# Optimization experiments

Measured on AMD Instinct MI355X. Metric: run time of the kernel, lower is better.

The kernel has to match this reference:

```python
import jax, jax.numpy as jnp
import numpy as np
import math

B, S, HID = 2, 1024, 2048
NH, HD = 16, 128
STREAM_R, SELECT_R, RECENT_R = 0.02, 0.06, 0.08
FF = 0.9  # forgetting factor
ROPE_BASE = 10000.0


def setup_inputs() -> dict:
    key = jax.random.key(0)
    ks = jax.random.split(key, 5)
    return {
        "hidden_states": jax.random.normal(ks[0], (B, S, HID), dtype=jnp.float32),
        "wq": jax.random.normal(ks[1], (HID, HID), dtype=jnp.float32) * 0.02,
        "wk": jax.random.normal(ks[2], (HID, HID), dtype=jnp.float32) * 0.02,
        "wv": jax.random.normal(ks[3], (HID, HID), dtype=jnp.float32) * 0.02,
        "wo": jax.random.normal(ks[4], (HID, HID), dtype=jnp.float32) * 0.02,
    }


def _rope_tables(seq_len, dim):
    inv_freq = 1.0 / (ROPE_BASE ** (jnp.arange(0, dim, 2, dtype=jnp.float32) / dim))
    freqs = jnp.outer(jnp.arange(seq_len, dtype=jnp.float32), inv_freq)  # [S, D/2]
    emb = jnp.concatenate([freqs, freqs], axis=-1)  # [S, D]
    return jnp.cos(emb), jnp.sin(emb)


def _rotate_half(x):
    x1, x2 = jnp.split(x, 2, axis=-1)
    return jnp.concatenate([-x2, x1], axis=-1)


def a2s_base_mask(attn_weights, sb, selb, rb, ff):
    # attn_weights: [B,H,S,S] (causal mask already added). Returns bool keep-mask [B,H,S,S].
    Bv, Hv, Sq, Sk = attn_weights.shape
    scores = jax.nn.softmax(attn_weights.astype(jnp.float32), axis=-1)  # [B,H,S,S]
    cb = sb + selb + rb  # cache budget
    # EMA warmup over first cb rows: sum_i ff^(cb-1-i) * scores[i]
    w = ff ** jnp.arange(cb - 1, -1, -1, dtype=jnp.float32)
    select0 = jnp.einsum('t,bhts->bhs', w, scores[:, :, :cb, :])
    mask0 = jnp.ones((Bv, Hv, Sk), dtype=bool)
    pos = jnp.arange(Sk)

    xs_scores = jnp.moveaxis(scores[:, :, cb:Sk - 1, :], 2, 0)  # [T,B,H,S]
    ts = jnp.arange(cb, Sk - 1, dtype=jnp.int32)

    def step(carry, inp):
        sel, m = carry
        sc, t = inp
        cur = sc * m
        cur = cur / jnp.sum(cur, axis=-1, keepdims=True)
        sel = ff * sel + cur
        local = t - rb
        # argmin over window [sb : local+1]; outside -> +inf (evicted entries already +inf)
        win = jnp.where((pos >= sb) & (pos <= local), sel, jnp.inf)
        mi = jnp.argmin(win, axis=-1)  # [B,H], first-min like torch
        evict = pos == mi[..., None]  # [B,H,S] one-hot bool
        sel = jnp.where(evict, jnp.inf, sel)
        m_new = m & ~evict
        return (sel, m_new), m_new

    _, rows = jax.lax.scan(step, (select0, mask0), (xs_scores, ts))
    head = jnp.ones((Bv, Hv, cb + 1, Sk), dtype=bool)  # rows 0..cb stay all-True
    tail = jnp.moveaxis(rows, 0, 2)  # rows cb+1..S-1
    return jnp.concatenate([head, tail], axis=2)


def reference(hidden_states, wq, wk, wv, wo):
    sb = math.floor(STREAM_R * S + 0.5)
    selb = math.floor(SELECT_R * S + 0.5)
    rb = math.floor(RECENT_R * S + 0.5)

    q = (hidden_states @ wq).reshape(B, S, NH, HD).transpose(0, 2, 1, 3)
    k = (hidden_states @ wk).reshape(B, S, NH, HD).transpose(0, 2, 1, 3)
    v = (hidden_states @ wv).reshape(B, S, NH, HD).transpose(0, 2, 1, 3)

    cos, sin = _rope_tables(S, HD)  # [S,HD]
    q = q * cos + _rotate_half(q) * sin
    k = k * cos + _rotate_half(k) * sin

    attn = jnp.einsum('bhqd,bhkd->bhqk', q, k) / math.sqrt(HD)
    mask_val = jnp.finfo(jnp.float32).min
    causal = jnp.where(jnp.tril(jnp.ones((S, S), dtype=bool)), 0.0, mask_val)[None, None]
    attn = jnp.maximum(attn + causal, mask_val)

    keep = a2s_base_mask(jax.lax.stop_gradient(attn), sb, selb, rb, FF)
    attn = jnp.where(keep, attn, mask_val)  # torch.min(attention_mask) == mask_val

    probs = jax.nn.softmax(attn.astype(jnp.float32), axis=-1).astype(q.dtype)
    out = jnp.einsum('bhqk,bhkd->bhqd', probs, v)
    out = out.transpose(0, 2, 1, 3).reshape(B, S, HID)
    return out @ wo
```

## Files before the change

kernel.cpp:

```cpp
#include <hip/hip_runtime.h>
#include <math.h>

#define Bb    2
#define Ss    1024
#define HIDd  2048
#define NHh   16
#define HDd   128
#define SBc   20
#define SELBc 61
#define RBc   82
#define CBc   163
#define FFf   0.9f
#define MASKVAL (-3.4028234663852886e38f)
#define NBH   (Bb*NHh)
#define NROWS (NBH*Ss)

typedef __attribute__((ext_vector_type(8))) short short8;
typedef __attribute__((ext_vector_type(4))) float f32x4;

__device__ __forceinline__ unsigned short f2b(float f) {
    unsigned u = __float_as_uint(f);
    u = (u + 0x7FFFu + ((u >> 16) & 1u)) >> 16;
    return (unsigned short)u;
}
__device__ __forceinline__ float b2f(unsigned short h) {
    return __uint_as_float((unsigned)h << 16);
}

#if defined(__has_builtin)
#if __has_builtin(__builtin_amdgcn_global_load_lds)
#define USE_GLD 1
#endif
#endif

__device__ __forceinline__ void gload16(const void* g, void* l) {
#ifdef USE_GLD
    __builtin_amdgcn_global_load_lds(
        (const __attribute__((address_space(1))) void*)g,
        (__attribute__((address_space(3))) void*)l, 16, 0, 0);
#else
    *(short8*)l = *(const short8*)g;
#endif
}

__global__ __launch_bounds__(256) void conv_split(const float* __restrict__ x,
                                                  unsigned short* __restrict__ yh,
                                                  unsigned short* __restrict__ yl, int n4)
{
    int i = blockIdx.x * 256 + threadIdx.x;
    if (i >= n4) return;
    float4 v = ((const float4*)x)[i];
    ushort4 h, l;
    h.x = f2b(v.x); l.x = f2b(v.x - b2f(h.x));
    h.y = f2b(v.y); l.y = f2b(v.y - b2f(h.y));
    h.z = f2b(v.z); l.z = f2b(v.z - b2f(h.z));
    h.w = f2b(v.w); l.w = f2b(v.w - b2f(h.w));
    ((ushort4*)yh)[i] = h;
    ((ushort4*)yl)[i] = l;
}

__global__ __launch_bounds__(256) void tconv_all(const float* __restrict__ wq,
                                                 const float* __restrict__ wk,
                                                 const float* __restrict__ wv,
                                                 const float* __restrict__ wo,
                                                 unsigned short* __restrict__ wqth,
                                                 unsigned short* __restrict__ wqtl,
                                                 unsigned short* __restrict__ wkth,
                                                 unsigned short* __restrict__ wktl,
                                                 unsigned short* __restrict__ wvt,
                                                 unsigned short* __restrict__ wot)
{
    __shared__ float T[64][65];
    const int z = blockIdx.z;
    const float* W = (z == 0) ? wq : (z == 1) ? wk : (z == 2) ? wv : wo;
    int n0 = blockIdx.x * 64, k0 = blockIdx.y * 64;
    int tid = threadIdx.x;
    int rr = tid >> 4, cc = (tid & 15) * 4;
#pragma unroll
    for (int p = 0; p < 4; ++p) {
        int r = rr + p * 16;
        float4 x = *(const float4*)&W[(size_t)(k0 + r) * HIDd + n0 + cc];
        T[r][cc] = x.x; T[r][cc + 1] = x.y; T[r][cc + 2] = x.z; T[r][cc + 3] = x.w;
    }
    __syncthreads();
    if (z < 2) {
        unsigned short* Wth = z ? wkth : wqth;
        unsigned short* Wtl = z ? wktl : wqtl;
#pragma unroll
        for (int p = 0; p < 4; ++p) {
            int rn = rr + p * 16;
            float v0 = T[cc][rn], v1 = T[cc + 1][rn], v2 = T[cc + 2][rn], v3 = T[cc + 3][rn];
            ushort4 h, l;
            h.x = f2b(v0); l.x = f2b(v0 - b2f(h.x));
            h.y = f2b(v1); l.y = f2b(v1 - b2f(h.y));
            h.z = f2b(v2); l.z = f2b(v2 - b2f(h.z));
            h.w = f2b(v3); l.w = f2b(v3 - b2f(h.w));
            *(ushort4*)&Wth[(size_t)(n0 + rn) * HIDd + k0 + cc] = h;
            *(ushort4*)&Wtl[(size_t)(n0 + rn) * HIDd + k0 + cc] = l;
        }
    } else {
        unsigned short* Wt = (z == 2) ? wvt : wot;
#pragma unroll
        for (int p = 0; p < 4; ++p) {
            int rn = rr + p * 16;
            ushort4 o;
            o.x = f2b(T[cc][rn]);     o.y = f2b(T[cc + 1][rn]);
            o.z = f2b(T[cc + 2][rn]); o.w = f2b(T[cc + 3][rn]);
            *(ushort4*)&Wt[(size_t)(n0 + rn) * HIDd + k0 + cc] = o;
        }
    }
}

__global__ __launch_bounds__(256) void gemm_qkv(const unsigned short* __restrict__ hsh,
                                                const unsigned short* __restrict__ hsl,
                                                const unsigned short* __restrict__ wqth,
                                                const unsigned short* __restrict__ wqtl,
                                                const unsigned short* __restrict__ wkth,
                                                const unsigned short* __restrict__ wktl,
                                                const unsigned short* __restrict__ wvt,
                                                float* __restrict__ qf,
                                                float* __restrict__ kf,
                                                float* __restrict__ vf)
{
    __shared__ unsigned short AsH[128 * 32], AsL[128 * 32];
    __shared__ unsigned short BsH[128 * 32], BsL[128 * 32];
    const int tid = threadIdx.x;
    const int region = blockIdx.x >> 4;
    const int bn = (blockIdx.x & 15) * 128;
    const int bm = blockIdx.y * 128;
    const int K = HIDd;
    const int lane = tid & 63, wid = tid >> 6;
    const int wr = (wid >> 1) * 64, wc = (wid & 1) * 64;
    const int lm = lane & 15, lk = (lane >> 4) * 8;
    const int lr = (lane >> 4) * 4;

    f32x4 acc[4][4];
#pragma unroll
    for (int mi = 0; mi < 4; ++mi)
#pragma unroll
        for (int ni = 0; ni < 4; ++ni) acc[mi][ni] = 0.0f;

    if (region < 2) {
        const unsigned short* Bh = region ? wkth : wqth;
        const unsigned short* Bl = region ? wktl : wqtl;
        float* C = region ? kf : qf;
        for (int k0 = 0; k0 < K; k0 += 32) {
#pragma unroll
            for (int l = 0; l < 2; ++l) {
                int L = tid + l * 256;
                int row = L >> 2, c8 = (L & 3) * 8;
                size_t ga = (size_t)(bm + row) * K + k0 + c8;
                size_t gb = (size_t)(bn + row) * K + k0 + c8;
                gload16(&hsh[ga], &AsH[L * 8]);
                gload16(&hsl[ga], &AsL[L * 8]);
                gload16(&Bh[gb], &BsH[L * 8]);
                gload16(&Bl[gb], &BsL[L * 8]);
            }
            __syncthreads();
            short8 ah[4], al[4], bh[4], bl[4];
#pragma unroll
            for (int mi = 0; mi < 4; ++mi) {
                ah[mi] = *(short8*)&AsH[(wr + mi * 16 + lm) * 32 + lk];
                al[mi] = *(short8*)&AsL[(wr + mi * 16 + lm) * 32 + lk];
            }
#pragma unroll
            for (int ni = 0; ni < 4; ++ni) {
                bh[ni] = *(short8*)&BsH[(wc + ni * 16 + lm) * 32 + lk];
                bl[ni] = *(short8*)&BsL[(wc + ni * 16 + lm) * 32 + lk];
            }
#pragma unroll
            for (int mi = 0; mi < 4; ++mi)
#pragma unroll
                for (int ni = 0; ni < 4; ++ni) {
                    acc[mi][ni] = __builtin_amdgcn_mfma_f32_16x16x32_bf16(ah[mi], bh[ni], acc[mi][ni], 0, 0, 0);
                    acc[mi][ni] = __builtin_amdgcn_mfma_f32_16x16x32_bf16(ah[mi], bl[ni], acc[mi][ni], 0, 0, 0);
                    acc[mi][ni] = __builtin_amdgcn_mfma_f32_16x16x32_bf16(al[mi], bh[ni], acc[mi][ni], 0, 0, 0);
                }
            __syncthreads();
        }
#pragma unroll
        for (int mi = 0; mi < 4; ++mi)
#pragma unroll
            for (int ni = 0; ni < 4; ++ni)
#pragma unroll
                for (int r = 0; r < 4; ++r) {
                    int m = bm + wr + mi * 16 + lr + r;
                    int n = bn + wc + ni * 16 + lm;
                    int b_ = m / Ss, s_ = m % Ss;
                    int h_ = n / HDd, d_ = n % HDd;
                    C[(size_t)((b_ * NHh + h_) * Ss + s_) * HDd + d_] = acc[mi][ni][r];
                }
    } else {
        for (int k0 = 0; k0 < K; k0 += 32) {
#pragma unroll
            for (int l = 0; l < 2; ++l) {
                int L = tid + l * 256;
                int row = L >> 2, c8 = (L & 3) * 8;
                gload16(&hsh[(size_t)(bm + row) * K + k0 + c8], &AsH[L * 8]);
                gload16(&wvt[(size_t)(bn + row) * K + k0 + c8], &BsH[L * 8]);
            }
            __syncthreads();
            short8 af[4], bf[4];
#pragma unroll
            for (int mi = 0; mi < 4; ++mi) af[mi] = *(short8*)&AsH[(wr + mi * 16 + lm) * 32 + lk];
#pragma unroll
            for (int ni = 0; ni < 4; ++ni) bf[ni] = *(short8*)&BsH[(wc + ni * 16 + lm) * 32 + lk];
#pragma unroll
            for (int mi = 0; mi < 4; ++mi)
#pragma unroll
                for (int ni = 0; ni < 4; ++ni)
                    acc[mi][ni] = __builtin_amdgcn_mfma_f32_16x16x32_bf16(af[mi], bf[ni], acc[mi][ni], 0, 0, 0);
            __syncthreads();
        }
#pragma unroll
        for (int mi = 0; mi < 4; ++mi)
#pragma unroll
            for (int ni = 0; ni < 4; ++ni)
#pragma unroll
                for (int r = 0; r < 4; ++r) {
                    int m = bm + wr + mi * 16 + lr + r;
                    int n = bn + wc + ni * 16 + lm;
                    int b_ = m / Ss, s_ = m % Ss;
                    int h_ = n / HDd, d_ = n % HDd;
                    vf[(size_t)((b_ * NHh + h_) * Ss + s_) * HDd + d_] = acc[mi][ni][r];
                }
    }
}

__global__ __launch_bounds__(256) void gemm_bf16t(const unsigned short* __restrict__ A,
                                                  const unsigned short* __restrict__ Bt,
                                                  float* __restrict__ C,
                                                  int M, int N, int K)
{
    __shared__ unsigned short As[128 * 32];
    __shared__ unsigned short Bs[128 * 32];
    const int tid = threadIdx.x;
    const int bm = blockIdx.y * 128, bn = blockIdx.x * 128;
    const int lane = tid & 63, wid = tid >> 6;
    const int wr = (wid >> 1) * 64, wc = (wid & 1) * 64;
    const int lm = lane & 15, lk = (lane >> 4) * 8;

    f32x4 acc[4][4];
#pragma unroll
    for (int mi = 0; mi < 4; ++mi)
#pragma unroll
        for (int ni = 0; ni < 4; ++ni) acc[mi][ni] = 0.0f;

    for (int k0 = 0; k0 < K; k0 += 32) {
#pragma unroll
        for (int l = 0; l < 2; ++l) {
            int L = tid + l * 256;
            int row = L >> 2, c8 = (L & 3) * 8;
            gload16(&A[(size_t)(bm + row) * K + k0 + c8], &As[L * 8]);
            gload16(&Bt[(size_t)(bn + row) * K + k0 + c8], &Bs[L * 8]);
        }
        __syncthreads();
        short8 af[4], bf[4];
#pragma unroll
        for (int mi = 0; mi < 4; ++mi) af[mi] = *(short8*)&As[(wr + mi * 16 + lm) * 32 + lk];
#pragma unroll
        for (int ni = 0; ni < 4; ++ni) bf[ni] = *(short8*)&Bs[(wc + ni * 16 + lm) * 32 + lk];
#pragma unroll
        for (int mi = 0; mi < 4; ++mi)
#pragma unroll
            for (int ni = 0; ni < 4; ++ni)
                acc[mi][ni] = __builtin_amdgcn_mfma_f32_16x16x32_bf16(af[mi], bf[ni], acc[mi][ni], 0, 0, 0);
        __syncthreads();
    }
    const int lr = (lane >> 4) * 4;
#pragma unroll
    for (int mi = 0; mi < 4; ++mi)
#pragma unroll
        for (int ni = 0; ni < 4; ++ni)
#pragma unroll
            for (int r = 0; r < 4; ++r) {
                int m = bm + wr + mi * 16 + lr + r;
                int n = bn + wc + ni * 16 + lm;
                C[(size_t)m * N + n] = acc[mi][ni][r];
            }
}

__global__ __launch_bounds__(64) void rope_qk_split(const float* __restrict__ q,
                                                    const float* __restrict__ k,
                                                    unsigned short* __restrict__ qh,
                                                    unsigned short* __restrict__ ql,
                                                    unsigned short* __restrict__ kh,
                                                    unsigned short* __restrict__ kl)
{
    int idx = blockIdx.x;
    int s = idx % Ss;
    int d = threadIdx.x;
    float inv = powf(10000.0f, -2.0f * (float)d / 128.0f);
    float fr = (float)s * inv;
    float c = cosf(fr), sn = sinf(fr);
    size_t base = (size_t)idx * HDd;
    float q1 = q[base + d], q2 = q[base + d + 64];
    float k1 = k[base + d], k2 = k[base + d + 64];
    float qa = q1 * c - q2 * sn, qbv = q2 * c + q1 * sn;
    float ka = k1 * c - k2 * sn, kbv = k2 * c + k1 * sn;
    unsigned short h;
    h = f2b(qa);  qh[base + d]      = h; ql[base + d]      = f2b(qa  - b2f(h));
    h = f2b(qbv); qh[base + d + 64] = h; ql[base + d + 64] = f2b(qbv - b2f(h));
    h = f2b(ka);  kh[base + d]      = h; kl[base + d]      = f2b(ka  - b2f(h));
    h = f2b(kbv); kh[base + d + 64] = h; kl[base + d + 64] = f2b(kbv - b2f(h));
}

__global__ __launch_bounds__(256) void attn_qk_split(const unsigned short* __restrict__ qh,
                                                     const unsigned short* __restrict__ ql,
                                                     const unsigned short* __restrict__ kh,
                                                     const unsigned short* __restrict__ kl,
                                                     float* __restrict__ attn)
{
    const int bh = blockIdx.z;
    const int bm = blockIdx.y * 128, bn = blockIdx.x * 128;
    const int tid = threadIdx.x;

    if (blockIdx.x > blockIdx.y) return;

    float* C = attn + (size_t)bh * Ss * Ss;
    const size_t hb = (size_t)bh * Ss * HDd;
    const unsigned short* Ah = qh + hb;
    const unsigned short* Al = ql + hb;
    const unsigned short* Bh = kh + hb;
    const unsigned short* Bl = kl + hb;

    __shared__ unsigned short AsH[128 * 32], AsL[128 * 32];
    __shared__ unsigned short BsH[128 * 32], BsL[128 * 32];
    const int lane = tid & 63, wid = tid >> 6;
    const int wr = (wid >> 1) * 64, wc = (wid & 1) * 64;
    const int lm = lane & 15, lk = (lane >> 4) * 8;

    f32x4 acc[4][4];
#pragma unroll
    for (int mi = 0; mi < 4; ++mi)
#pragma unroll
        for (int ni = 0; ni < 4; ++ni) acc[mi][ni] = 0.0f;

    for (int k0 = 0; k0 < HDd; k0 += 32) {
#pragma unroll
        for (int l = 0; l < 2; ++l) {
            int L = tid + l * 256;
            int row = L >> 2, c8 = (L & 3) * 8;
            size_t ga = (size_t)(bm + row) * HDd + k0 + c8;
            size_t gb = (size_t)(bn + row) * HDd + k0 + c8;
            gload16(&Ah[ga], &AsH[L * 8]);
            gload16(&Al[ga], &AsL[L * 8]);
            gload16(&Bh[gb], &BsH[L * 8]);
            gload16(&Bl[gb], &BsL[L * 8]);
        }
        __syncthreads();
        short8 ah[4], al[4], bh2[4], bl2[4];
#pragma unroll
        for (int mi = 0; mi < 4; ++mi) {
            ah[mi] = *(short8*)&AsH[(wr + mi * 16 + lm) * 32 + lk];
            al[mi] = *(short8*)&AsL[(wr + mi * 16 + lm) * 32 + lk];
        }
#pragma unroll
        for (int ni = 0; ni < 4; ++ni) {
            bh2[ni] = *(short8*)&BsH[(wc + ni * 16 + lm) * 32 + lk];
            bl2[ni] = *(short8*)&BsL[(wc + ni * 16 + lm) * 32 + lk];
        }
#pragma unroll
        for (int mi = 0; mi < 4; ++mi)
#pragma unroll
            for (int ni = 0; ni < 4; ++ni) {
                acc[mi][ni] = __builtin_amdgcn_mfma_f32_16x16x32_bf16(ah[mi], bh2[ni], acc[mi][ni], 0, 0, 0);
                acc[mi][ni] = __builtin_amdgcn_mfma_f32_16x16x32_bf16(ah[mi], bl2[ni], acc[mi][ni], 0, 0, 0);
                acc[mi][ni] = __builtin_amdgcn_mfma_f32_16x16x32_bf16(al[mi], bh2[ni], acc[mi][ni], 0, 0, 0);
            }
        __syncthreads();
    }
    const float scale = 0.08838834764831845f;
    const int lr = (lane >> 4) * 4;
#pragma unroll
    for (int mi = 0; mi < 4; ++mi)
#pragma unroll
        for (int ni = 0; ni < 4; ++ni)
#pragma unroll
            for (int r = 0; r < 4; ++r) {
                int sq = bm + wr + mi * 16 + lr + r;
                int sk = bn + wc + ni * 16 + lm;
                C[(size_t)sq * Ss + sk] = (sk <= sq) ? acc[mi][ni][r] * scale : MASKVAL;
            }
}

__global__ __launch_bounds__(256) void softmax_rows(float* __restrict__ attn)
{
    int row = blockIdx.x;
    int r = row & (Ss - 1);
    float4* a4 = (float4*)(attn + (size_t)row * Ss);
    int tid = threadIdx.x;
    bool act = (tid * 4 <= r);
    float4 x = make_float4(MASKVAL, MASKVAL, MASKVAL, MASKVAL);
    if (act) x = a4[tid];
    float m = fmaxf(fmaxf(x.x, x.y), fmaxf(x.z, x.w));
#pragma unroll
    for (int off = 32; off; off >>= 1) m = fmaxf(m, __shfl_xor(m, off));
    __shared__ float red[4];
    if ((tid & 63) == 0) red[tid >> 6] = m;
    __syncthreads();
    float mm = fmaxf(fmaxf(red[0], red[1]), fmaxf(red[2], red[3]));
    float e0 = expf(x.x - mm), e1 = expf(x.y - mm);
    float e2 = expf(x.z - mm), e3 = expf(x.w - mm);
    float s = e0 + e1 + e2 + e3;
#pragma unroll
    for (int off = 32; off; off >>= 1) s += __shfl_xor(s, off);
    __shared__ float red2[4];
    if ((tid & 63) == 0) red2[tid >> 6] = s;
    __syncthreads();
    float inv = 1.0f / (red2[0] + red2[1] + red2[2] + red2[3]);
    a4[tid] = make_float4(e0 * inv, e1 * inv, e2 * inv, e3 * inv);
}

template<int CTRL>
__device__ __forceinline__ int dpp_i(int x) {
    return __builtin_amdgcn_update_dpp(0, x, CTRL, 0xF, 0xF, true);
}
__device__ __forceinline__ float wave_sum64(float x) {
    x += __int_as_float(dpp_i<0xB1>(__float_as_int(x)));
    x += __int_as_float(dpp_i<0x4E>(__float_as_int(x)));
    x += __int_as_float(dpp_i<0x141>(__float_as_int(x)));
    x += __int_as_float(dpp_i<0x140>(__float_as_int(x)));
    int xi = __float_as_int(x);
    float a = __int_as_float(__builtin_amdgcn_readlane(xi, 0));
    float b = __int_as_float(__builtin_amdgcn_readlane(xi, 16));
    float c = __int_as_float(__builtin_amdgcn_readlane(xi, 32));
    float d = __int_as_float(__builtin_amdgcn_readlane(xi, 48));
    return (a + c) + (b + d);
}

__device__ __forceinline__ unsigned long long u64min(unsigned long long a, unsigned long long b) {
    return a < b ? a : b;
}
template<int CTRL>
__device__ __forceinline__ unsigned long long dpp64(unsigned long long x) {
    int lo = (int)(unsigned)x;
    int hi = (int)(unsigned)(x >> 32);
    unsigned l2 = (unsigned)dpp_i<CTRL>(lo);
    unsigned h2 = (unsigned)dpp_i<CTRL>(hi);
    return ((unsigned long long)h2 << 32) | (unsigned long long)l2;
}
__device__ __forceinline__ unsigned long long wave_min64k(unsigned long long x) {
    x = u64min(x, dpp64<0xB1>(x));
    x = u64min(x, dpp64<0x4E>(x));
    x = u64min(x, dpp64<0x141>(x));
    x = u64min(x, dpp64<0x140>(x));
    int lo = (int)(unsigned)x;
    int hi = (int)(unsigned)(x >> 32);
    unsigned long long a = ((unsigned long long)(unsigned)__builtin_amdgcn_readlane(hi, 0)  << 32) |
                           (unsigned long long)(unsigned)__builtin_amdgcn_readlane(lo, 0);
    unsigned long long b = ((unsigned long long)(unsigned)__builtin_amdgcn_readlane(hi, 16) << 32) |
                           (unsigned long long)(unsigned)__builtin_amdgcn_readlane(lo, 16);
    unsigned long long c = ((unsigned long long)(unsigned)__builtin_amdgcn_readlane(hi, 32) << 32) |
                           (unsigned long long)(unsigned)__builtin_amdgcn_readlane(lo, 32);
    unsigned long long d = ((unsigned long long)(unsigned)__builtin_amdgcn_readlane(hi, 48) << 32) |
                           (unsigned long long)(unsigned)__builtin_amdgcn_readlane(lo, 48);
    return u64min(u64min(a, b), u64min(c, d));
}

__device__ __forceinline__ float f4c(float4 v, int i) {
    return i == 0 ? v.x : (i == 1 ? v.y : (i == 2 ? v.z : v.w));
}

template<int NC, int NCL>
__device__ __forceinline__ void scan_step(int t, int lane,
                                          const float4* __restrict__ A4,
                                          unsigned char* __restrict__ KP,
                                          float4 (&rb)[4],
                                          float (&sel)[4][4],
                                          float (&mf)[4][4])
{
    const float INFv = __int_as_float(0x7f800000);
    float4 a[NC];
#pragma unroll
    for (int jj = 0; jj < NC; ++jj) a[jj] = rb[jj];
    int tp = t + 4; if (tp > Ss - 1) tp = Ss - 1;
#pragma unroll
    for (int jj = 0; jj < NCL; ++jj) rb[jj] = A4[tp * 256 + jj * 64 + lane];

    float lsum = 0.0f;
#pragma unroll
    for (int jj = 0; jj < NC; ++jj) {
        float c0 = a[jj].x * mf[jj][0], c1 = a[jj].y * mf[jj][1];
        float c2 = a[jj].z * mf[jj][2], c3 = a[jj].w * mf[jj][3];
        lsum += (c0 + c1) + (c2 + c3);
    }
    float tot = wave_sum64(lsum);
    float inv = 1.0f / tot;

    const int local = t - RBc;
    const int base = lane * 4;
    const bool ge = (base >= SBc);

    unsigned long long kmin = 0xFFFFFFFFFFFFFFFFull;
#pragma unroll
    for (int jj = 0; jj < NC; ++jj) {
        unsigned long long kk[4];
#pragma unroll
        for (int i = 0; i < 4; ++i) {
            float sv = fmaf(FFf, sel[jj][i], f4c(a[jj], i) * inv);
            sel[jj][i] = sv;
            int s = jj * 256 + base + i;
            bool win = (s <= local) && (jj > 0 || ge);
            unsigned hi = win ? __float_as_uint(sv) : 0x7f800000u;
            kk[i] = ((unsigned long long)hi << 32) | (unsigned long long)(unsigned)s;
        }
        unsigned long long cm = u64min(u64min(kk[0], kk[1]), u64min(kk[2], kk[3]));
        kmin = u64min(kmin, cm);
    }
    kmin = wave_min64k(kmin);
    const int besti = (int)(unsigned)(kmin & 0xFFFFFFFFull);

#pragma unroll
    for (int jj = 0; jj < NC; ++jj)
#pragma unroll
        for (int i = 0; i < 4; ++i) {
            int s = jj * 256 + base + i;
            bool e = (s == besti);
            sel[jj][i] = e ? INFv : sel[jj][i];
            mf[jj][i]  = e ? 0.0f : mf[jj][i];
        }

    uchar4* kp4 = (uchar4*)(KP + (size_t)(t + 1) * Ss);
#pragma unroll
    for (int jj = 0; jj < NC; ++jj) {
        uchar4 kb;
        kb.x = (unsigned char)mf[jj][0];
        kb.y = (unsigned char)mf[jj][1];
        kb.z = (unsigned char)mf[jj][2];
        kb.w = (unsigned char)mf[jj][3];
        kp4[jj * 64 + lane] = kb;
    }
}

__global__ __launch_bounds__(64) void scan_kernel5(const float* __restrict__ scores,
                                                   unsigned char* __restrict__ keep)
{
    int bh = blockIdx.x;
    int lane = threadIdx.x;
    const float4* A4 = (const float4*)(scores + (size_t)bh * Ss * Ss);
    unsigned char* KP = keep + (size_t)bh * Ss * Ss;

    float sel[4][4];
    float mf[4][4];
#pragma unroll
    for (int jj = 0; jj < 4; ++jj)
#pragma unroll
        for (int i = 0; i < 4; ++i) { sel[jj][i] = 0.0f; mf[jj][i] = 1.0f; }

    float4 w0 = A4[0 * 256 + lane];
    float4 w1 = A4[1 * 256 + lane];
    float4 w2 = A4[2 * 256 + lane];
    float4 w3 = A4[3 * 256 + lane];
#define WSTEP(W, NEXT)                                                       \
    do {                                                                     \
        float4 _a = W;                                                       \
        W = A4[(NEXT) * 256 + lane];                                         \
        sel[0][0] = fmaf(FFf, sel[0][0], _a.x);                              \
        sel[0][1] = fmaf(FFf, sel[0][1], _a.y);                              \
        sel[0][2] = fmaf(FFf, sel[0][2], _a.z);                              \
        sel[0][3] = fmaf(FFf, sel[0][3], _a.w);                              \
    } while (0)
    for (int r = 0; r < 160; r += 4) {
        WSTEP(w0, r + 4); WSTEP(w1, r + 5); WSTEP(w2, r + 6); WSTEP(w3, r + 7);
    }
#undef WSTEP
    {
        float4 tl[3] = { w0, w1, w2 };
#pragma unroll
        for (int u = 0; u < 3; ++u) {
            sel[0][0] = fmaf(FFf, sel[0][0], tl[u].x);
            sel[0][1] = fmaf(FFf, sel[0][1], tl[u].y);
            sel[0][2] = fmaf(FFf, sel[0][2], tl[u].z);
            sel[0][3] = fmaf(FFf, sel[0][3], tl[u].w);
        }
    }

    float4 rb[4][4];
#pragma unroll
    for (int slot = 0; slot < 4; ++slot)
        rb[slot][0] = A4[(163 + slot) * 256 + lane];

    for (int t0 = 163; t0 < 255; t0 += 4) {
        scan_step<1, 2>(t0 + 0, lane, A4, KP, rb[0], sel, mf);
        scan_step<1, 2>(t0 + 1, lane, A4, KP, rb[1], sel, mf);
        scan_step<1, 2>(t0 + 2, lane, A4, KP, rb[2], sel, mf);
        scan_step<1, 2>(t0 + 3, lane, A4, KP, rb[3], sel, mf);
    }
    for (int t0 = 255; t0 < 511; t0 += 4) {
        scan_step<2, 3>(t0 + 0, lane, A4, KP, rb[0], sel, mf);
        scan_step<2, 3>(t0 + 1, lane, A4, KP, rb[1], sel, mf);
        scan_step<2, 3>(t0 + 2, lane, A4, KP, rb[2], sel, mf);
        scan_step<2, 3>(t0 + 3, lane, A4, KP, rb[3], sel, mf);
    }
    for (int t0 = 511; t0 < 767; t0 += 4) {
        scan_step<3, 4>(t0 + 0, lane, A4, KP, rb[0], sel, mf);
        scan_step<3, 4>(t0 + 1, lane, A4, KP, rb[1], sel, mf);
        scan_step<3, 4>(t0 + 2, lane, A4, KP, rb[2], sel, mf);
        scan_step<3, 4>(t0 + 3, lane, A4, KP, rb[3], sel, mf);
    }
    for (int t0 = 767; t0 < 1023; t0 += 4) {
        scan_step<4, 4>(t0 + 0, lane, A4, KP, rb[0], sel, mf);
        scan_step<4, 4>(t0 + 1, lane, A4, KP, rb[1], sel, mf);
        scan_step<4, 4>(t0 + 2, lane, A4, KP, rb[2], sel, mf);
        scan_step<4, 4>(t0 + 3, lane, A4, KP, rb[3], sel, mf);
    }
}

__global__ __launch_bounds__(256) void pv_renorm(const float* __restrict__ scores,
                                                 const unsigned char* __restrict__ keep,
                                                 const float* __restrict__ v,
                                                 unsigned short* __restrict__ ctxb)
{
    int bh = blockIdx.z;
    int b_ = bh / NHh, h_ = bh % NHh;
    const float* P = scores + (size_t)bh * Ss * Ss;
    const unsigned char* KPm = keep + (size_t)bh * Ss * Ss;
    const float* V = v + (size_t)bh * Ss * HDd;
    int bm = blockIdx.y * 64, bn = blockIdx.x * 64;
    int tid = threadIdx.x, tx = tid & 15, ty = tid >> 4;
    __shared__ float As[16][68];
    __shared__ float Bs[16][64];
    float acc[4][4] = {};
    float rs[4] = {};
    int kend = bm + 64;
    for (int k0 = 0; k0 < kend; k0 += 16) {
#pragma unroll
        for (int l = 0; l < 4; ++l) {
            int idx = tid + l * 256;
            int r = idx >> 4, c = idx & 15;
            int row = bm + r;
            float p = P[(size_t)row * Ss + k0 + c];
            if (row > CBc && !KPm[(size_t)row * Ss + k0 + c]) p = 0.0f;
            As[c][r] = p;
        }
#pragma unroll
        for (int l = 0; l < 4; ++l) {
            int idx = tid + l * 256;
            int r = idx >> 6, c = idx & 63;
            Bs[r][c] = V[(size_t)(k0 + r) * HDd + bn + c];
        }
        __syncthreads();
#pragma unroll
        for (int kk = 0; kk < 16; ++kk) {
            float4 av = *(const float4*)&As[kk][ty * 4];
            float4 bv = *(const float4*)&Bs[kk][tx * 4];
            float a[4] = { av.x, av.y, av.z, av.w };
            float b[4] = { bv.x, bv.y, bv.z, bv.w };
#pragma unroll
            for (int i = 0; i < 4; ++i) rs[i] += a[i];
#pragma unroll
            for (int i = 0; i < 4; ++i)
#pragma unroll
                for (int j = 0; j < 4; ++j)
                    acc[i][j] = fmaf(a[i], b[j], acc[i][j]);
        }
        __syncthreads();
    }
#pragma unroll
    for (int i = 0; i < 4; ++i) {
        float inv = 1.0f / rs[i];
        int sq = bm + ty * 4 + i;
#pragma unroll
        for (int j = 0; j < 4; ++j) {
            int d = bn + tx * 4 + j;
            ctxb[(size_t)(b_ * Ss + sq) * HIDd + h_ * HDd + d] = f2b(acc[i][j] * inv);
        }
    }
}

extern "C" void kernel_launch(void* const* d_in, const int* in_sizes, int n_in,
                              void* d_out, int out_size, void* d_ws, size_t ws_size,
                              hipStream_t stream)
{
    const float* hs = (const float*)d_in[0];
    const float* wq = (const float*)d_in[1];
    const float* wk = (const float*)d_in[2];
    const float* wv = (const float*)d_in[3];
    const float* wo = (const float*)d_in[4];
    float* out = (float*)d_out;

    float* ws = (float*)d_ws;
    size_t off = 0;
    float* qf   = ws + off; off += (size_t)NBH * Ss * HDd;
    float* kf   = ws + off; off += (size_t)NBH * Ss * HDd;
    float* vf   = ws + off; off += (size_t)NBH * Ss * HDd;
    float* attn = ws + off; off += (size_t)NBH * Ss * Ss;
    unsigned char* keep = (unsigned char*)(ws + off); off += (size_t)NBH * Ss * Ss / 4;
    unsigned short* wot = (unsigned short*)(ws + off); off += (size_t)HIDd * HIDd / 2;

    unsigned short* hsh  = (unsigned short*)(attn);
    unsigned short* hsl  = (unsigned short*)(attn + 2u * 1024 * 1024);
    unsigned short* wqth = (unsigned short*)(attn + 4u * 1024 * 1024);
    unsigned short* wqtl = (unsigned short*)(attn + 6u * 1024 * 1024);
    unsigned short* wkth = (unsigned short*)(attn + 8u * 1024 * 1024);
    unsigned short* wktl = (unsigned short*)(attn + 10u * 1024 * 1024);
    unsigned short* wvt  = (unsigned short*)(attn + 12u * 1024 * 1024);
    unsigned short* qh = (unsigned short*)keep;
    unsigned short* ql = (unsigned short*)(keep + 8u * 1024 * 1024);
    unsigned short* kh = (unsigned short*)(keep + 16u * 1024 * 1024);
    unsigned short* kl = (unsigned short*)(keep + 24u * 1024 * 1024);
    unsigned short* ctxb = (unsigned short*)qf;

    dim3 blk(256);
    const int M = Bb * Ss;

    conv_split<<<dim3((M * HIDd / 4 + 255) / 256), blk, 0, stream>>>(hs, hsh, hsl, M * HIDd / 4);

    tconv_all<<<dim3(HIDd / 64, HIDd / 64, 4), blk, 0, stream>>>(
        wq, wk, wv, wo, wqth, wqtl, wkth, wktl, wvt, wot);

    gemm_qkv<<<dim3(48, M / 128), blk, 0, stream>>>(
        hsh, hsl, wqth, wqtl, wkth, wktl, wvt, qf, kf, vf);

    rope_qk_split<<<dim3(NBH * Ss), dim3(64), 0, stream>>>(qf, kf, qh, ql, kh, kl);

    attn_qk_split<<<dim3(Ss / 128, Ss / 128, NBH), blk, 0, stream>>>(qh, ql, kh, kl, attn);

    softmax_rows<<<dim3(NROWS), blk, 0, stream>>>(attn);

    scan_kernel5<<<dim3(NBH), dim3(64), 0, stream>>>(attn, keep);

    pv_renorm<<<dim3(HDd / 64, Ss / 64, NBH), blk, 0, stream>>>(attn, keep, vf, ctxb);

    gemm_bf16t<<<dim3(HIDd / 128, M / 128), blk, 0, stream>>>(ctxb, wot, out, M, HIDd, HIDd);
}
```

Before: 974.9 us.

## Fuse RoPE and bf16 hi/lo split into QKV GEMM epilogue; skip masked diagonal MFMAs

The Q/K projection GEMM now applies rotary embedding and writes the bf16 high/low split directly in its epilogue. The two head-dim halves are exchanged through shared memory, so the fp32 q/k intermediates and the separate rope_qk_split launch go away. Separately, diagonal blocks of the QK^T kernel skip MFMA sub-tiles that lie entirely above the causal diagonal. This trades extra epilogue work and a barrier in the GEMM for less global memory traffic and one fewer launch. Only half the warps do the rope epilogue, which may leave the other half idle.

Result: slower. 1.434 ms (+47.1%).

```diff
diff --git a/kernel.cpp b/kernel.cpp
--- a/kernel.cpp
+++ b/kernel.cpp
@@ -118,12 +118,17 @@
                                                 const unsigned short* __restrict__ wkth,
                                                 const unsigned short* __restrict__ wktl,
                                                 const unsigned short* __restrict__ wvt,
-                                                float* __restrict__ qf,
-                                                float* __restrict__ kf,
+                                                unsigned short* __restrict__ qhp,
+                                                unsigned short* __restrict__ qlp,
+                                                unsigned short* __restrict__ khp,
+                                                unsigned short* __restrict__ klp,
                                                 float* __restrict__ vf)
 {
-    __shared__ unsigned short AsH[128 * 32], AsL[128 * 32];
-    __shared__ unsigned short BsH[128 * 32], BsL[128 * 32];
+    __shared__ unsigned short SM[4 * 128 * 32];
+    unsigned short* AsH = SM;
+    unsigned short* AsL = SM + 128 * 32;
+    unsigned short* BsH = SM + 2 * 128 * 32;
+    unsigned short* BsL = SM + 3 * 128 * 32;
     const int tid = threadIdx.x;
     const int region = blockIdx.x >> 4;
     const int bn = (blockIdx.x & 15) * 128;
@@ -143,7 +148,6 @@
     if (region < 2) {
         const unsigned short* Bh = region ? wkth : wqth;
         const unsigned short* Bl = region ? wktl : wqtl;
-        float* C = region ? kf : qf;
         for (int k0 = 0; k0 < K; k0 += 32) {
 #pragma unroll
             for (int l = 0; l < 2; ++l) {
@@ -178,18 +182,53 @@
                 }
             __syncthreads();
         }
-#pragma unroll
-        for (int mi = 0; mi < 4; ++mi)
-#pragma unroll
-            for (int ni = 0; ni < 4; ++ni)
+        unsigned short* Ho = region ? khp : qhp;
+        unsigned short* Lo = region ? klp : qlp;
+        float* Lx = (float*)SM;
+        if (wc) {
+#pragma unroll
+            for (int mi = 0; mi < 4; ++mi)
+#pragma unroll
+                for (int ni = 0; ni < 4; ++ni)
+#pragma unroll
+                    for (int r = 0; r < 4; ++r) {
+                        int row = wr + mi * 16 + lr + r;
+                        int dc = ni * 16 + lm;
+                        Lx[row * 64 + dc] = acc[mi][ni][r];
+                    }
+        }
+        __syncthreads();
+        if (!wc) {
+            float invt[4];
+#pragma unroll
+            for (int ni = 0; ni < 4; ++ni) {
+                int d = ni * 16 + lm;
+                invt[ni] = powf(10000.0f, -2.0f * (float)d / 128.0f);
+            }
+            const int hh = bn >> 7;
+#pragma unroll
+            for (int mi = 0; mi < 4; ++mi)
 #pragma unroll
                 for (int r = 0; r < 4; ++r) {
-                    int m = bm + wr + mi * 16 + lr + r;
-                    int n = bn + wc + ni * 16 + lm;
-                    int b_ = m / Ss, s_ = m % Ss;
-                    int h_ = n / HDd, d_ = n % HDd;
-                    C[(size_t)((b_ * NHh + h_) * Ss + s_) * HDd + d_] = acc[mi][ni][r];
+                    int row = wr + mi * 16 + lr + r;
+                    int m = bm + row;
+                    int b_ = m >> 10, s_ = m & (Ss - 1);
+                    size_t gb = ((size_t)(b_ * NHh + hh) * Ss + s_) * HDd;
+#pragma unroll
+                    for (int ni = 0; ni < 4; ++ni) {
+                        int d = ni * 16 + lm;
+                        float q1 = acc[mi][ni][r];
+                        float q2 = Lx[row * 64 + d];
+                        float fr = (float)s_ * invt[ni];
+                        float c = cosf(fr), sn = sinf(fr);
+                        float qa  = q1 * c - q2 * sn;
+                        float qbv = q2 * c + q1 * sn;
+                        unsigned short h;
+                        h = f2b(qa);  Ho[gb + d]      = h; Lo[gb + d]      = f2b(qa  - b2f(h));
+                        h = f2b(qbv); Ho[gb + d + 64] = h; Lo[gb + d + 64] = f2b(qbv - b2f(h));
+                    }
                 }
+        }
     } else {
         for (int k0 = 0; k0 < K; k0 += 32) {
 #pragma unroll
@@ -280,31 +319,6 @@
             }
 }
 
-__global__ __launch_bounds__(64) void rope_qk_split(const float* __restrict__ q,
-                                                    const float* __restrict__ k,
-                                                    unsigned short* __restrict__ qh,
-                                                    unsigned short* __restrict__ ql,
-                                                    unsigned short* __restrict__ kh,
-                                                    unsigned short* __restrict__ kl)
-{
-    int idx = blockIdx.x;
-    int s = idx % Ss;
-    int d = threadIdx.x;
-    float inv = powf(10000.0f, -2.0f * (float)d / 128.0f);
-    float fr = (float)s * inv;
-    float c = cosf(fr), sn = sinf(fr);
-    size_t base = (size_t)idx * HDd;
-    float q1 = q[base + d], q2 = q[base + d + 64];
-    float k1 = k[base + d], k2 = k[base + d + 64];
-    float qa = q1 * c - q2 * sn, qbv = q2 * c + q1 * sn;
-    float ka = k1 * c - k2 * sn, kbv = k2 * c + k1 * sn;
-    unsigned short h;
-    h = f2b(qa);  qh[base + d]      = h; ql[base + d]      = f2b(qa  - b2f(h));
-    h = f2b(qbv); qh[base + d + 64] = h; ql[base + d + 64] = f2b(qbv - b2f(h));
-    h = f2b(ka);  kh[base + d]      = h; kl[base + d]      = f2b(ka  - b2f(h));
-    h = f2b(kbv); kh[base + d + 64] = h; kl[base + d + 64] = f2b(kbv - b2f(h));
-}
-
 __global__ __launch_bounds__(256) void attn_qk_split(const unsigned short* __restrict__ qh,
                                                      const unsigned short* __restrict__ ql,
                                                      const unsigned short* __restrict__ kh,
@@ -316,6 +330,7 @@
     const int tid = threadIdx.x;
 
     if (blockIdx.x > blockIdx.y) return;
+    const bool diag = (blockIdx.x == blockIdx.y);
 
     float* C = attn + (size_t)bh * Ss * Ss;
     const size_t hb = (size_t)bh * Ss * HDd;
@@ -364,6 +379,7 @@
         for (int mi = 0; mi < 4; ++mi)
 #pragma unroll
             for (int ni = 0; ni < 4; ++ni) {
+                if (diag && (wc + ni * 16 > wr + mi * 16 + 15)) continue;
                 acc[mi][ni] = __builtin_amdgcn_mfma_f32_16x16x32_bf16(ah[mi], bh2[ni], acc[mi][ni], 0, 0, 0);
                 acc[mi][ni] = __builtin_amdgcn_mfma_f32_16x16x32_bf16(ah[mi], bl2[ni], acc[mi][ni], 0, 0, 0);
                 acc[mi][ni] = __builtin_amdgcn_mfma_f32_16x16x32_bf16(al[mi], bh2[ni], acc[mi][ni], 0, 0, 0);
@@ -701,6 +717,7 @@
     unsigned short* kh = (unsigned short*)(keep + 16u * 1024 * 1024);
     unsigned short* kl = (unsigned short*)(keep + 24u * 1024 * 1024);
     unsigned short* ctxb = (unsigned short*)qf;
+    (void)kf;
 
     dim3 blk(256);
     const int M = Bb * Ss;
@@ -711,9 +728,7 @@
         wq, wk, wv, wo, wqth, wqtl, wkth, wktl, wvt, wot);
 
     gemm_qkv<<<dim3(48, M / 128), blk, 0, stream>>>(
-        hsh, hsl, wqth, wqtl, wkth, wktl, wvt, qf, kf, vf);
-
-    rope_qk_split<<<dim3(NBH * Ss), dim3(64), 0, stream>>>(qf, kf, qh, ql, kh, kl);
+        hsh, hsl, wqth, wqtl, wkth, wktl, wvt, qh, ql, kh, kl, vf);
 
     attn_qk_split<<<dim3(Ss / 128, Ss / 128, NBH), blk, 0, stream>>>(qh, ql, kh, kl, attn);
 
```
